# Kernel optimization log

Hardware: AMD Instinct MI355X
Metric: run time of the kernel (lower is better)

The kernel has to match this reference:

```python
import jax, jax.numpy as jnp
import numpy as np

N_NODES = 50000
N_EDGES = 800000
D_FEAT = 64          # per-node feature dim
HIDDEN = 128         # fc1 output dim; fc1 input = 2*D_FEAT


def setup_inputs() -> dict:
    key = jax.random.key(0)
    k1, k2, k3 = jax.random.split(key, 3)
    x = jax.random.normal(k1, (N_NODES, D_FEAT), dtype=jnp.float32)
    edge_index = jax.random.randint(k2, (2, N_EDGES), 0, N_NODES, dtype=jnp.int64)
    # fc1: Linear(2*D_FEAT, HIDDEN); torch Linear weight is [out, in]
    W = jax.random.normal(k3, (HIDDEN, 2 * D_FEAT), dtype=jnp.float32) * (1.0 / np.sqrt(2 * D_FEAT))
    b = jnp.zeros((HIDDEN,), dtype=jnp.float32)
    return {"x": x, "edge_index": edge_index, "W": W, "b": b}


def reference(x, edge_index, W, b):
    # Gather source-node features along edges, sum-scatter to destinations.
    src, dst = edge_index[0], edge_index[1]
    gathered = x[src]  # [E, D_FEAT] -- dominant memory traffic
    neigh = jax.ops.segment_sum(gathered, dst, num_segments=x.shape[0])  # [N, D_FEAT]
    # Concat self features with aggregated neighbor features, then Linear+ReLU.
    h = jnp.concatenate([x, neigh], axis=-1)          # [N, 2*D_FEAT]
    out = jax.nn.relu(h @ W.T + b)                    # [N, HIDDEN]
    return out
```

## Files before the change

kernel.cpp:

```cpp
#include <hip/hip_runtime.h>

#define N_NODES 50000
#define N_EDGES 800000
#define DFEAT 64
#define HID 128
#define NBKT 16
#define NPB1 3200
#define CAP_C 57344
#define NRCH 56
#define SUBB 50
#define NSUB 800
#define CAP_S 1536

#define XB_BLOCKS 3125
#define WB_BLOCKS 16
#define EB_BLOCKS 782

typedef __bf16 bf16x8 __attribute__((ext_vector_type(8)));
typedef float f32x4 __attribute__((ext_vector_type(4)));

__device__ inline unsigned short f2bf(float f) {
  unsigned u = __float_as_uint(f);
  return (unsigned short)((u + 0x7FFFu + ((u >> 16) & 1u)) >> 16);
}
__device__ inline float bf2f(unsigned short h) {
  return __uint_as_float(((unsigned)h) << 16);
}

__global__ __launch_bounds__(256) void k_prep(const float* __restrict__ x,
                                              const float* __restrict__ W,
                                              const int* __restrict__ ei,
                                              unsigned short* __restrict__ xb,
                                              unsigned short* __restrict__ Wb,
                                              int* __restrict__ ccnt,
                                              unsigned int* __restrict__ coarse) {
  int bid = blockIdx.x;
  if (bid < XB_BLOCKS) {
    int t = bid * 256 + threadIdx.x;
    float4 v = *(const float4*)&x[t * 4];
    ushort4 o = {f2bf(v.x), f2bf(v.y), f2bf(v.z), f2bf(v.w)};
    *(ushort4*)&xb[t * 4] = o;
    return;
  }
  bid -= XB_BLOCKS;
  if (bid < WB_BLOCKS) {
    int t = bid * 256 + threadIdx.x;
    float4 v = *(const float4*)&W[t * 4];
    ushort4 o = {f2bf(v.x), f2bf(v.y), f2bf(v.z), f2bf(v.w)};
    *(ushort4*)&Wb[t * 4] = o;
    return;
  }
  bid -= WB_BLOCKS;
  __shared__ int lcnt[NBKT];
  __shared__ int lbase[NBKT];
  const int tid = threadIdx.x;
  if (tid < NBKT) lcnt[tid] = 0;
  __syncthreads();

  int e0 = (bid * 256 + tid) * 4;
  bool valid = e0 < N_EDGES;
  int bkt[4], rank[4];
  unsigned int pk[4];
  if (valid) {
    int4 s4 = *(const int4*)&ei[e0];
    int4 d4 = *(const int4*)&ei[N_EDGES + e0];
    int ss[4] = {s4.x, s4.y, s4.z, s4.w};
    int dd[4] = {d4.x, d4.y, d4.z, d4.w};
#pragma unroll
    for (int i = 0; i < 4; ++i) {
      bkt[i] = dd[i] / NPB1;
      pk[i] = ((unsigned)dd[i] << 16) | (unsigned)ss[i];
    }
#pragma unroll
    for (int i = 0; i < 4; ++i) rank[i] = atomicAdd(&lcnt[bkt[i]], 1);
  }
  __syncthreads();
  if (tid < NBKT) lbase[tid] = atomicAdd(&ccnt[tid], lcnt[tid]);
  __syncthreads();
  if (valid) {
#pragma unroll
    for (int i = 0; i < 4; ++i) {
      int pos = lbase[bkt[i]] + rank[i];
      if (pos < CAP_C) coarse[bkt[i] * CAP_C + pos] = pk[i];
    }
  }
}

__global__ __launch_bounds__(256) void k_refine(const unsigned int* __restrict__ coarse,
                                                const int* __restrict__ ccnt,
                                                int* __restrict__ subcnt,
                                                unsigned int* __restrict__ sub) {
  __shared__ int lcnt[SUBB];
  __shared__ int lbase[SUBB];
  const int tid = threadIdx.x;
  const int b = blockIdx.x / NRCH;
  const int c = blockIdx.x % NRCH;

  if (tid < SUBB) lcnt[tid] = 0;
  __syncthreads();

  int cnt = ccnt[b];
  cnt = cnt < CAP_C ? cnt : CAP_C;
  const unsigned int* cb = &coarse[(size_t)b * CAP_C];
  int idx0 = c * 1024 + tid * 4;

  unsigned p[4];
  int sl[4], rk[4];
  bool v[4];
#pragma unroll
  for (int i = 0; i < 4; ++i) {
    v[i] = (idx0 + i) < cnt;
    p[i] = v[i] ? cb[idx0 + i] : 0u;
  }
#pragma unroll
  for (int i = 0; i < 4; ++i) {
    if (v[i]) {
      int d = (int)(p[i] >> 16);
      sl[i] = (d >> 6) - b * SUBB;
      rk[i] = atomicAdd(&lcnt[sl[i]], 1);
    }
  }
  __syncthreads();
  if (tid < SUBB) lbase[tid] = atomicAdd(&subcnt[b * SUBB + tid], lcnt[tid]);
  __syncthreads();
#pragma unroll
  for (int i = 0; i < 4; ++i) {
    if (v[i]) {
      int d = (int)(p[i] >> 16);
      int pos = lbase[sl[i]] + rk[i];
      if (pos < CAP_S)
        sub[(size_t)(b * SUBB + sl[i]) * CAP_S + pos] =
            ((unsigned)(d & 63) << 16) | (p[i] & 0xffffu);
    }
  }
}

__global__ __launch_bounds__(1024) void k_pullsub(const unsigned short* __restrict__ xb,
                                                  const int* __restrict__ subcnt,
                                                  const unsigned int* __restrict__ sub,
                                                  unsigned short* __restrict__ nbf) {
  __shared__ unsigned int q[CAP_S];
  __shared__ unsigned int sq[CAP_S];
  __shared__ int lcnt[64];
  __shared__ int lbase[65];

  const int tid = threadIdx.x;
  const int sb = blockIdx.x;
  const int nb = sb * 64;

  if (tid < 64) lcnt[tid] = 0;

  int cnt = subcnt[sb];
  cnt = cnt < CAP_S ? cnt : CAP_S;
  const unsigned int* qb = &sub[(size_t)sb * CAP_S];
  for (int i = tid; i < cnt; i += 1024) q[i] = qb[i];
  __syncthreads();

  int myrank[2], myidx[2], nloc = 0;
  for (int i = tid; i < cnt; i += 1024) {
    int rel = (int)(q[i] >> 16);
    myrank[nloc] = atomicAdd(&lcnt[rel], 1);
    myidx[nloc] = i;
    ++nloc;
  }
  __syncthreads();
  if (tid < 64) {
    int v = lcnt[tid];
    int inc = v;
#pragma unroll
    for (int o = 1; o < 64; o <<= 1) {
      int u = __shfl_up(inc, o);
      if (tid >= o) inc += u;
    }
    lbase[tid] = inc - v;
    if (tid == 63) lbase[64] = inc;
  }
  __syncthreads();
  for (int k = 0; k < nloc; ++k) {
    unsigned e = q[myidx[k]];
    sq[lbase[e >> 16] + myrank[k]] = e;
  }
  __syncthreads();

  const int wave = tid >> 6;
  const int lane = tid & 63;
  const int half = lane >> 5;
  const int l31 = lane & 31;
  const unsigned int* xu = (const unsigned int*)xb;

#pragma unroll
  for (int i2 = 0; i2 < 4; ++i2) {
    int n = wave * 4 + i2;
    int beg = lbase[n], end = lbase[n + 1];
    float s0x = 0.f, s0y = 0.f, s1x = 0.f, s1y = 0.f,
          s2x = 0.f, s2y = 0.f, s3x = 0.f, s3y = 0.f;
    int j = beg + half;
    for (; j + 6 < end; j += 8) {
      unsigned e0 = sq[j], e1 = sq[j + 2], e2 = sq[j + 4], e3 = sq[j + 6];
      unsigned v0 = xu[(e0 & 0xffffu) * 32 + l31];
      unsigned v1 = xu[(e1 & 0xffffu) * 32 + l31];
      unsigned v2 = xu[(e2 & 0xffffu) * 32 + l31];
      unsigned v3 = xu[(e3 & 0xffffu) * 32 + l31];
      s0x += bf2f((unsigned short)(v0 & 0xffffu)); s0y += bf2f((unsigned short)(v0 >> 16));
      s1x += bf2f((unsigned short)(v1 & 0xffffu)); s1y += bf2f((unsigned short)(v1 >> 16));
      s2x += bf2f((unsigned short)(v2 & 0xffffu)); s2y += bf2f((unsigned short)(v2 >> 16));
      s3x += bf2f((unsigned short)(v3 & 0xffffu)); s3y += bf2f((unsigned short)(v3 >> 16));
    }
    for (; j < end; j += 2) {
      unsigned e = sq[j];
      unsigned v = xu[(e & 0xffffu) * 32 + l31];
      s0x += bf2f((unsigned short)(v & 0xffffu));
      s0y += bf2f((unsigned short)(v >> 16));
    }
    float sx = (s0x + s1x) + (s2x + s3x);
    float sy = (s0y + s1y) + (s2y + s3y);
    sx += __shfl_xor(sx, 32);
    sy += __shfl_xor(sy, 32);
    int node = nb + n;
    if (half == 0 && node < N_NODES) {
      unsigned o = (unsigned)f2bf(sx) | ((unsigned)f2bf(sy) << 16);
      ((unsigned int*)nbf)[node * 32 + l31] = o;
    }
  }
}

__global__ __launch_bounds__(256) void k_fc(const unsigned short* __restrict__ xb,
                                            const unsigned short* __restrict__ nbf,
                                            const unsigned short* __restrict__ Wb,
                                            const float* __restrict__ bv,
                                            float* __restrict__ out) {
  const int tid = threadIdx.x;
  const int wave = tid >> 6;
  const int lane = tid & 63;
  const int l15 = lane & 15;
  const int quad = lane >> 4;
  const int node0 = blockIdx.x * 64 + wave * 16;

  int anode = node0 + l15;
  if (anode >= N_NODES) anode = N_NODES - 1;
  const unsigned short* hx = xb + (size_t)anode * DFEAT;
  const unsigned short* hn = nbf + (size_t)anode * DFEAT;

  bf16x8 a0 = *(const bf16x8*)(hx + quad * 8);
  bf16x8 a1 = *(const bf16x8*)(hx + 32 + quad * 8);
  bf16x8 a2 = *(const bf16x8*)(hn + quad * 8);
  bf16x8 a3 = *(const bf16x8*)(hn + 32 + quad * 8);

  f32x4 acc[8];
#pragma unroll
  for (int nt = 0; nt < 8; ++nt) acc[nt] = (f32x4){0.f, 0.f, 0.f, 0.f};

#pragma unroll
  for (int nt = 0; nt < 8; ++nt) {
    const unsigned short* wr = Wb + (size_t)(nt * 16 + l15) * (2 * DFEAT) + quad * 8;
    bf16x8 b0 = *(const bf16x8*)(wr);
    bf16x8 b1 = *(const bf16x8*)(wr + 32);
    bf16x8 b2 = *(const bf16x8*)(wr + 64);
    bf16x8 b3 = *(const bf16x8*)(wr + 96);
    acc[nt] = __builtin_amdgcn_mfma_f32_16x16x32_bf16(a0, b0, acc[nt], 0, 0, 0);
    acc[nt] = __builtin_amdgcn_mfma_f32_16x16x32_bf16(a1, b1, acc[nt], 0, 0, 0);
    acc[nt] = __builtin_amdgcn_mfma_f32_16x16x32_bf16(a2, b2, acc[nt], 0, 0, 0);
    acc[nt] = __builtin_amdgcn_mfma_f32_16x16x32_bf16(a3, b3, acc[nt], 0, 0, 0);
  }

#pragma unroll
  for (int nt = 0; nt < 8; ++nt) {
    float bias = bv[nt * 16 + l15];
#pragma unroll
    for (int r = 0; r < 4; ++r) {
      int node = node0 + quad * 4 + r;
      if (node < N_NODES) {
        float v = acc[nt][r] + bias;
        out[(size_t)node * HID + nt * 16 + l15] = v > 0.f ? v : 0.f;
      }
    }
  }
}

extern "C" void kernel_launch(void* const* d_in, const int* in_sizes, int n_in,
                              void* d_out, int out_size, void* d_ws, size_t ws_size,
                              hipStream_t stream) {
  const float* x = (const float*)d_in[0];
  const int* ei = (const int*)d_in[1];
  const float* W = (const float*)d_in[2];
  const float* b = (const float*)d_in[3];
  float* out = (float*)d_out;

  char* ws = (char*)d_ws;
  int* ccnt            = (int*)ws;            ws += 256;
  int* subcnt          = (int*)ws;            ws += 3328;
  unsigned int* coarse = (unsigned int*)ws;   ws += (size_t)NBKT * CAP_C * 4;
  unsigned int* sub    = (unsigned int*)ws;   ws += (size_t)NSUB * CAP_S * 4;
  unsigned short* xb   = (unsigned short*)ws; ws += (size_t)N_NODES * DFEAT * 2;
  unsigned short* Wb   = (unsigned short*)ws; ws += (size_t)HID * 2 * DFEAT * 2;
  unsigned short* nbf  = (unsigned short*)ws; ws += (size_t)N_NODES * DFEAT * 2;

  hipMemsetAsync(ccnt, 0, 256 + 3328, stream);

  k_prep<<<XB_BLOCKS + WB_BLOCKS + EB_BLOCKS, 256, 0, stream>>>(
      x, W, ei, xb, Wb, ccnt, coarse);
  k_refine<<<NBKT * NRCH, 256, 0, stream>>>(coarse, ccnt, subcnt, sub);
  k_pullsub<<<(N_NODES + 63) / 64, 1024, 0, stream>>>(xb, subcnt, sub, nbf);
  k_fc<<<(N_NODES + 63) / 64, 256, 0, stream>>>(xb, nbf, Wb, b, out);
}
```

Measured before the change: 138.5 us.

## Fuse neighbor aggregation with FC, use per-block coarse slots, drop memset

Merges the pull-aggregation kernel and the MFMA linear layer into one kernel. The aggregated neighbor features stay in shared memory instead of taking a round trip through a global bf16 buffer. The coarse bucketing now gives each edge block fixed slots per bucket, which removes the global atomic base counter, and the subcount zeroing moves into the prep kernel so the hipMemsetAsync can go. This saves one launch, a global write and read of neighbor features, and a memset, at the cost of 16 waves per block doing the FC and a fixed per-block slot cap that could silently drop edges on skewed inputs.

```diff
diff --git a/kernel.cpp b/kernel.cpp
--- a/kernel.cpp
+++ b/kernel.cpp
@@ -6,11 +6,14 @@
 #define HID 128
 #define NBKT 16
 #define NPB1 3200
-#define CAP_C 57344
+#define SLOTS 112
+#define CAPB (782 * SLOTS)
+#define SEGS 14
 #define NRCH 56
 #define SUBB 50
 #define NSUB 800
 #define CAP_S 1536
+#define NSTR 66
 
 #define XB_BLOCKS 3125
 #define WB_BLOCKS 16
@@ -32,7 +35,8 @@
                                               const int* __restrict__ ei,
                                               unsigned short* __restrict__ xb,
                                               unsigned short* __restrict__ Wb,
-                                              int* __restrict__ ccnt,
+                                              int* __restrict__ subcnt,
+                                              int* __restrict__ pcnt,
                                               unsigned int* __restrict__ coarse) {
   int bid = blockIdx.x;
   if (bid < XB_BLOCKS) {
@@ -48,19 +52,18 @@
     float4 v = *(const float4*)&W[t * 4];
     ushort4 o = {f2bf(v.x), f2bf(v.y), f2bf(v.z), f2bf(v.w)};
     *(ushort4*)&Wb[t * 4] = o;
+    int z = bid * 50 + threadIdx.x;
+    if (threadIdx.x < 50 && z < NSUB) subcnt[z] = 0;
     return;
   }
   bid -= WB_BLOCKS;
   __shared__ int lcnt[NBKT];
-  __shared__ int lbase[NBKT];
   const int tid = threadIdx.x;
   if (tid < NBKT) lcnt[tid] = 0;
   __syncthreads();
 
   int e0 = (bid * 256 + tid) * 4;
   bool valid = e0 < N_EDGES;
-  int bkt[4], rank[4];
-  unsigned int pk[4];
   if (valid) {
     int4 s4 = *(const int4*)&ei[e0];
     int4 d4 = *(const int4*)&ei[N_EDGES + e0];
@@ -68,79 +71,79 @@
     int dd[4] = {d4.x, d4.y, d4.z, d4.w};
 #pragma unroll
     for (int i = 0; i < 4; ++i) {
-      bkt[i] = dd[i] / NPB1;
-      pk[i] = ((unsigned)dd[i] << 16) | (unsigned)ss[i];
-    }
-#pragma unroll
-    for (int i = 0; i < 4; ++i) rank[i] = atomicAdd(&lcnt[bkt[i]], 1);
-  }
-  __syncthreads();
-  if (tid < NBKT) lbase[tid] = atomicAdd(&ccnt[tid], lcnt[tid]);
-  __syncthreads();
-  if (valid) {
-#pragma unroll
-    for (int i = 0; i < 4; ++i) {
-      int pos = lbase[bkt[i]] + rank[i];
-      if (pos < CAP_C) coarse[bkt[i] * CAP_C + pos] = pk[i];
-    }
+      int bkt = dd[i] / NPB1;
+      int rank = atomicAdd(&lcnt[bkt], 1);
+      if (rank < SLOTS)
+        coarse[(size_t)bkt * CAPB + bid * SLOTS + rank] =
+            ((unsigned)dd[i] << 16) | (unsigned)ss[i];
+    }
+  }
+  __syncthreads();
+  if (tid < NBKT) {
+    int c = lcnt[tid];
+    pcnt[bid * NBKT + tid] = c < SLOTS ? c : SLOTS;
   }
 }
 
 __global__ __launch_bounds__(256) void k_refine(const unsigned int* __restrict__ coarse,
-                                                const int* __restrict__ ccnt,
+                                                const int* __restrict__ pcnt,
                                                 int* __restrict__ subcnt,
                                                 unsigned int* __restrict__ sub) {
   __shared__ int lcnt[SUBB];
   __shared__ int lbase[SUBB];
+  __shared__ int scnt[SEGS];
   const int tid = threadIdx.x;
   const int b = blockIdx.x / NRCH;
   const int c = blockIdx.x % NRCH;
 
   if (tid < SUBB) lcnt[tid] = 0;
-  __syncthreads();
-
-  int cnt = ccnt[b];
-  cnt = cnt < CAP_C ? cnt : CAP_C;
-  const unsigned int* cb = &coarse[(size_t)b * CAP_C];
-  int idx0 = c * 1024 + tid * 4;
-
-  unsigned p[4];
-  int sl[4], rk[4];
-  bool v[4];
-#pragma unroll
-  for (int i = 0; i < 4; ++i) {
-    v[i] = (idx0 + i) < cnt;
-    p[i] = v[i] ? cb[idx0 + i] : 0u;
-  }
-#pragma unroll
-  for (int i = 0; i < 4; ++i) {
-    if (v[i]) {
-      int d = (int)(p[i] >> 16);
-      sl[i] = (d >> 6) - b * SUBB;
-      rk[i] = atomicAdd(&lcnt[sl[i]], 1);
+  if (tid < SEGS) {
+    int seg = c * SEGS + tid;
+    scnt[tid] = (seg < EB_BLOCKS) ? pcnt[seg * NBKT + b] : 0;
+  }
+  __syncthreads();
+
+  unsigned p[7];
+  int sl[7], rk[7];
+  bool v[7];
+#pragma unroll
+  for (int j = 0; j < 7; ++j) {
+    int idx = j * 256 + tid;
+    v[j] = false;
+    if (idx < SEGS * SLOTS) {
+      int seg = idx / SLOTS;
+      int off = idx % SLOTS;
+      if (off < scnt[seg]) {
+        p[j] = coarse[(size_t)b * CAPB + (c * SEGS + seg) * SLOTS + off];
+        sl[j] = ((int)(p[j] >> 16) >> 6) - b * SUBB;
+        rk[j] = atomicAdd(&lcnt[sl[j]], 1);
+        v[j] = true;
+      }
     }
   }
   __syncthreads();
   if (tid < SUBB) lbase[tid] = atomicAdd(&subcnt[b * SUBB + tid], lcnt[tid]);
   __syncthreads();
 #pragma unroll
-  for (int i = 0; i < 4; ++i) {
-    if (v[i]) {
-      int d = (int)(p[i] >> 16);
-      int pos = lbase[sl[i]] + rk[i];
+  for (int j = 0; j < 7; ++j) {
+    if (v[j]) {
+      int pos = lbase[sl[j]] + rk[j];
       if (pos < CAP_S)
-        sub[(size_t)(b * SUBB + sl[i]) * CAP_S + pos] =
-            ((unsigned)(d & 63) << 16) | (p[i] & 0xffffu);
-    }
-  }
-}
-
-__global__ __launch_bounds__(1024) void k_pullsub(const unsigned short* __restrict__ xb,
-                                                  const int* __restrict__ subcnt,
-                                                  const unsigned int* __restrict__ sub,
-                                                  unsigned short* __restrict__ nbf) {
+        sub[(size_t)(b * SUBB + sl[j]) * CAP_S + pos] =
+            ((p[j] & 0x3f0000u)) | (p[j] & 0xffffu);
+    }
+  }
+}
+
+__global__ __launch_bounds__(1024) void k_gnn(const unsigned short* __restrict__ xb,
+                                              const unsigned short* __restrict__ Wb,
+                                              const int* __restrict__ subcnt,
+                                              const unsigned int* __restrict__ sub,
+                                              const float* __restrict__ bv,
+                                              float* __restrict__ out) {
   __shared__ unsigned int q[CAP_S];
   __shared__ unsigned int sq[CAP_S];
+  __shared__ unsigned int ns_u[32 * NSTR];
   __shared__ int lcnt[64];
   __shared__ int lbase[65];
 
@@ -216,61 +219,63 @@
     float sy = (s0y + s1y) + (s2y + s3y);
     sx += __shfl_xor(sx, 32);
     sy += __shfl_xor(sy, 32);
-    int node = nb + n;
-    if (half == 0 && node < N_NODES) {
-      unsigned o = (unsigned)f2bf(sx) | ((unsigned)f2bf(sy) << 16);
-      ((unsigned int*)nbf)[node * 32 + l31] = o;
-    }
-  }
-}
-
-__global__ __launch_bounds__(256) void k_fc(const unsigned short* __restrict__ xb,
-                                            const unsigned short* __restrict__ nbf,
-                                            const unsigned short* __restrict__ Wb,
-                                            const float* __restrict__ bv,
-                                            float* __restrict__ out) {
-  const int tid = threadIdx.x;
-  const int wave = tid >> 6;
-  const int lane = tid & 63;
+    if (half == 0)
+      ns_u[l31 * NSTR + n] = (unsigned)f2bf(sx) | ((unsigned)f2bf(sy) << 16);
+  }
+  __syncthreads();
+
+  const int g = wave & 3;
+  const int o = wave >> 2;
   const int l15 = lane & 15;
   const int quad = lane >> 4;
-  const int node0 = blockIdx.x * 64 + wave * 16;
+  const int node0 = nb + g * 16;
 
   int anode = node0 + l15;
   if (anode >= N_NODES) anode = N_NODES - 1;
   const unsigned short* hx = xb + (size_t)anode * DFEAT;
-  const unsigned short* hn = nbf + (size_t)anode * DFEAT;
-
-  bf16x8 a0 = *(const bf16x8*)(hx + quad * 8);
-  bf16x8 a1 = *(const bf16x8*)(hx + 32 + quad * 8);
-  bf16x8 a2 = *(const bf16x8*)(hn + quad * 8);
-  bf16x8 a3 = *(const bf16x8*)(hn + 32 + quad * 8);
-
-  f32x4 acc[8];
-#pragma unroll
-  for (int nt = 0; nt < 8; ++nt) acc[nt] = (f32x4){0.f, 0.f, 0.f, 0.f};
-
-#pragma unroll
-  for (int nt = 0; nt < 8; ++nt) {
+
+  bf16x8 fa0 = *(const bf16x8*)(hx + quad * 8);
+  bf16x8 fa1 = *(const bf16x8*)(hx + 32 + quad * 8);
+  bf16x8 fa2, fa3;
+  {
+    int m = g * 16 + l15;
+    union { unsigned u[4]; bf16x8 v; } c2, c3;
+#pragma unroll
+    for (int i = 0; i < 4; ++i) {
+      c2.u[i] = ns_u[(quad * 4 + i) * NSTR + m];
+      c3.u[i] = ns_u[(16 + quad * 4 + i) * NSTR + m];
+    }
+    fa2 = c2.v;
+    fa3 = c3.v;
+  }
+
+  f32x4 accr[2];
+#pragma unroll
+  for (int t = 0; t < 2; ++t) accr[t] = (f32x4){0.f, 0.f, 0.f, 0.f};
+
+#pragma unroll
+  for (int t = 0; t < 2; ++t) {
+    int nt = o * 2 + t;
     const unsigned short* wr = Wb + (size_t)(nt * 16 + l15) * (2 * DFEAT) + quad * 8;
     bf16x8 b0 = *(const bf16x8*)(wr);
     bf16x8 b1 = *(const bf16x8*)(wr + 32);
     bf16x8 b2 = *(const bf16x8*)(wr + 64);
     bf16x8 b3 = *(const bf16x8*)(wr + 96);
-    acc[nt] = __builtin_amdgcn_mfma_f32_16x16x32_bf16(a0, b0, acc[nt], 0, 0, 0);
-    acc[nt] = __builtin_amdgcn_mfma_f32_16x16x32_bf16(a1, b1, acc[nt], 0, 0, 0);
-    acc[nt] = __builtin_amdgcn_mfma_f32_16x16x32_bf16(a2, b2, acc[nt], 0, 0, 0);
-    acc[nt] = __builtin_amdgcn_mfma_f32_16x16x32_bf16(a3, b3, acc[nt], 0, 0, 0);
-  }
-
-#pragma unroll
-  for (int nt = 0; nt < 8; ++nt) {
+    accr[t] = __builtin_amdgcn_mfma_f32_16x16x32_bf16(fa0, b0, accr[t], 0, 0, 0);
+    accr[t] = __builtin_amdgcn_mfma_f32_16x16x32_bf16(fa1, b1, accr[t], 0, 0, 0);
+    accr[t] = __builtin_amdgcn_mfma_f32_16x16x32_bf16(fa2, b2, accr[t], 0, 0, 0);
+    accr[t] = __builtin_amdgcn_mfma_f32_16x16x32_bf16(fa3, b3, accr[t], 0, 0, 0);
+  }
+
+#pragma unroll
+  for (int t = 0; t < 2; ++t) {
+    int nt = o * 2 + t;
     float bias = bv[nt * 16 + l15];
 #pragma unroll
     for (int r = 0; r < 4; ++r) {
       int node = node0 + quad * 4 + r;
       if (node < N_NODES) {
-        float v = acc[nt][r] + bias;
+        float v = accr[t][r] + bias;
         out[(size_t)node * HID + nt * 16 + l15] = v > 0.f ? v : 0.f;
       }
     }
@@ -287,19 +292,15 @@
   float* out = (float*)d_out;
 
   char* ws = (char*)d_ws;
-  int* ccnt            = (int*)ws;            ws += 256;
   int* subcnt          = (int*)ws;            ws += 3328;
-  unsigned int* coarse = (unsigned int*)ws;   ws += (size_t)NBKT * CAP_C * 4;
+  int* pcnt            = (int*)ws;            ws += (size_t)EB_BLOCKS * NBKT * 4;
+  unsigned int* coarse = (unsigned int*)ws;   ws += (size_t)NBKT * CAPB * 4;
   unsigned int* sub    = (unsigned int*)ws;   ws += (size_t)NSUB * CAP_S * 4;
   unsigned short* xb   = (unsigned short*)ws; ws += (size_t)N_NODES * DFEAT * 2;
   unsigned short* Wb   = (unsigned short*)ws; ws += (size_t)HID * 2 * DFEAT * 2;
-  unsigned short* nbf  = (unsigned short*)ws; ws += (size_t)N_NODES * DFEAT * 2;
-
-  hipMemsetAsync(ccnt, 0, 256 + 3328, stream);
 
   k_prep<<<XB_BLOCKS + WB_BLOCKS + EB_BLOCKS, 256, 0, stream>>>(
-      x, W, ei, xb, Wb, ccnt, coarse);
-  k_refine<<<NBKT * NRCH, 256, 0, stream>>>(coarse, ccnt, subcnt, sub);
-  k_pullsub<<<(N_NODES + 63) / 64, 1024, 0, stream>>>(xb, subcnt, sub, nbf);
-  k_fc<<<(N_NODES + 63) / 64, 256, 0, stream>>>(xb, nbf, Wb, b, out);
-}
+      x, W, ei, xb, Wb, subcnt, pcnt, coarse);
+  k_refine<<<NBKT * NRCH, 256, 0, stream>>>(coarse, pcnt, subcnt, sub);
+  k_gnn<<<(N_NODES + 63) / 64, 1024, 0, stream>>>(xb, Wb, subcnt, sub, b, out);
+}
```

Result: faster. 127.1 us (-8.3%).
